# Kernel tuning notes

Measured on AMD Instinct MI355X. Metric: run time of the kernel, lower is better.

## Reference

```python
import jax, jax.numpy as jnp
import numpy as np

NUM_HEADS = 16  # matches init_kwargs num_heads
ROPE_BASE = 10000.0


def _rope(x):
    # x: [B, H, T, d_k]; canonical interleaved rotary embedding
    d = x.shape[-1]
    T = x.shape[-2]
    inv_freq = 1.0 / (ROPE_BASE ** (jnp.arange(0, d, 2, dtype=jnp.float32) / d))  # [d/2]
    ang = jnp.arange(T, dtype=jnp.float32)[:, None] * inv_freq[None, :]  # [T, d/2]
    cos, sin = jnp.cos(ang), jnp.sin(ang)  # broadcast over B,H
    x1 = x[..., 0::2]
    x2 = x[..., 1::2]
    even = x1 * cos - x2 * sin
    odd = x1 * sin + x2 * cos
    return jnp.stack([even, odd], axis=-1).reshape(x.shape)


def setup_inputs() -> dict:
    key = jax.random.key(0)
    ks = jax.random.split(key, 5)
    B, T, D = 2, 2048, 2048
    s = 1.0 / np.sqrt(D)
    return {
        "x": jax.random.normal(ks[0], (B, T, D), dtype=jnp.float32),
        "Wkqv": jax.random.normal(ks[1], (D, 3 * D), dtype=jnp.float32) * s,
        "bkqv": jax.random.normal(ks[2], (3 * D,), dtype=jnp.float32) * 0.01,
        "Wo": jax.random.normal(ks[3], (D, D), dtype=jnp.float32) * s,
        "bo": jax.random.normal(ks[4], (D,), dtype=jnp.float32) * 0.01,
    }


def reference(x, Wkqv, bkqv, Wo, bo):
    B, T, D = x.shape
    H = NUM_HEADS
    d_k = D // H
    kqv = x @ Wkqv + bkqv  # [B, T, 3D]
    # split order per source: index 0 = K, 1 = Q, 2 = V
    k, q, v = jnp.split(kqv, 3, axis=-1)

    def heads(t):  # [B, T, D] -> [B, H, T, d_k]
        return t.reshape(B, T, H, d_k).transpose(0, 2, 1, 3)

    k, q, v = heads(k), heads(q), heads(v)
    k = _rope(k)
    q = _rope(q)
    scores = jnp.einsum('bhtd,bhTd->bhtT', q, k)  # [B, H, T, T]
    causal = jnp.triu(jnp.ones((T, T), dtype=bool), k=1)
    scores = jnp.where(causal, -jnp.inf, scores)
    attn = jax.nn.softmax(scores / jnp.sqrt(jnp.float32(d_k)), axis=-1)
    out = jnp.einsum('bhtT,bhTd->bhtd', attn, v)  # [B, H, T, d_k]
    out = out.transpose(0, 2, 1, 3).reshape(B, T, D)
    return out @ Wo + bo
```

## Files before the change

kernel.cpp:

```cpp
#include <hip/hip_runtime.h>
#include <cstdint>
#include <cstddef>

typedef __attribute__((ext_vector_type(4))) float  floatx4;
typedef __attribute__((ext_vector_type(8))) __bf16 bf16x8;
typedef __attribute__((ext_vector_type(4))) __bf16 bf16x4;

#define B_   2
#define T_   2048
#define D_   2048
#define H_   16
#define DK   128
#define BT_  (B_ * T_)
#define N3   (3 * D_)

__device__ __forceinline__ void async_copy16(const void* g, void* l) {
    __builtin_amdgcn_global_load_lds((const __attribute__((address_space(1))) void*)g,
                                     (__attribute__((address_space(3))) void*)l,
                                     16, 0, 0);
}

__global__ void cast_bf16_kernel(const float* __restrict__ in, __bf16* __restrict__ out, int n4) {
    int i = blockIdx.x * 256 + threadIdx.x;
    if (i >= n4) return;
    float4 v = ((const float4*)in)[i];
    bf16x4 o;
    o.x = (__bf16)v.x; o.y = (__bf16)v.y; o.z = (__bf16)v.z; o.w = (__bf16)v.w;
    ((bf16x4*)out)[i] = o;
}

__global__ void transcast_kernel(const float* __restrict__ in, __bf16* __restrict__ out, int R, int C) {
    __shared__ float tile[32][33];
    int c0 = blockIdx.x * 32, r0 = blockIdx.y * 32;
    int tx = threadIdx.x, ty = threadIdx.y;
#pragma unroll
    for (int j = 0; j < 32; j += 8)
        tile[ty + j][tx] = in[(size_t)(r0 + ty + j) * C + c0 + tx];
    __syncthreads();
#pragma unroll
    for (int j = 0; j < 32; j += 8)
        out[(size_t)(c0 + ty + j) * R + r0 + tx] = (__bf16)tile[tx][ty + j];
}

__global__ void vtrans_kernel(const __bf16* __restrict__ kqv, __bf16* __restrict__ VT) {
    __shared__ __bf16 tile[32][33];
    int bh = blockIdx.z; int b = bh >> 4, h = bh & 15;
    int t0 = blockIdx.x * 32, d0 = blockIdx.y * 32;
    int tx = threadIdx.x, ty = threadIdx.y;
#pragma unroll
    for (int j = 0; j < 32; j += 8)
        tile[ty + j][tx] = kqv[(size_t)(b * T_ + t0 + ty + j) * N3 + 2 * D_ + h * DK + d0 + tx];
    __syncthreads();
#pragma unroll
    for (int j = 0; j < 32; j += 8)
        VT[(size_t)(bh * DK + d0 + ty + j) * T_ + t0 + tx] = tile[tx][ty + j];
}

__global__ void rope_kernel(const __bf16* __restrict__ kqv,
                            __bf16* __restrict__ Kh, __bf16* __restrict__ Qh) {
    int idx = blockIdx.x * 256 + threadIdx.x;
    int i     = idx & 63;
    int t     = (idx >> 6) & (T_ - 1);
    int bh    = (idx >> 17) & 31;
    int which = idx >> 22;
    int b = bh >> 4, h = bh & 15;
    const __bf16* src = kqv + (size_t)(b * T_ + t) * N3 + which * D_ + h * DK + 2 * i;
    float x1 = (float)src[0], x2 = (float)src[1];
    float freq = exp2f((float)i * (-13.287712379549449f / 64.f));
    float ang = (float)t * freq;
    float sn, cn; sincosf(ang, &sn, &cn);
    float s = which ? 0.12751740f : 1.0f;
    __bf16* dst = (which ? Qh : Kh) + (size_t)(bh * T_ + t) * DK + 2 * i;
    dst[0] = (__bf16)((x1 * cn - x2 * sn) * s);
    dst[1] = (__bf16)((x1 * sn + x2 * cn) * s);
}

template <typename OutT>
__global__ __launch_bounds__(256)
void gemm_bt(const __bf16* __restrict__ A, const __bf16* __restrict__ BTm,
             const float* __restrict__ bias, OutT* __restrict__ C,
             int M, int N, int K) {
    __shared__ __align__(16) __bf16 As[128 * 64];
    __shared__ __align__(16) __bf16 Bs[128 * 64];
    const int tid  = threadIdx.x;
    const int lane = tid & 63;
    const int wave = tid >> 6;
    const int quad = lane >> 4;
    const int l16  = lane & 15;
    const int m0 = blockIdx.y * 128;
    const int n0 = blockIdx.x * 128;
    const int wm = (wave & 1) * 64;
    const int wn = (wave >> 1) * 64;

    const floatx4 z4 = {0.f, 0.f, 0.f, 0.f};
    floatx4 acc[4][4];
#pragma unroll
    for (int i = 0; i < 4; ++i)
#pragma unroll
        for (int j = 0; j < 4; ++j) acc[i][j] = z4;

    int           sOff[4];
    const __bf16* gA[4];
    const __bf16* gB[4];
#pragma unroll
    for (int i = 0; i < 4; ++i) {
        int s = i * 256 + tid;
        int row = s >> 3, cs = s & 7;
        int gc = cs ^ (row & 7);
        sOff[i] = s * 8;
        gA[i] = A   + (size_t)(m0 + row) * K + gc * 8;
        gB[i] = BTm + (size_t)(n0 + row) * K + gc * 8;
    }

    for (int kt = 0; kt < K; kt += 64) {
        __syncthreads();
#pragma unroll
        for (int i = 0; i < 4; ++i) {
            async_copy16(gA[i] + kt, As + sOff[i]);
            async_copy16(gB[i] + kt, Bs + sOff[i]);
        }
        __syncthreads();
#pragma unroll
        for (int ks2 = 0; ks2 < 2; ++ks2) {
            bf16x8 af[4], bf[4];
#pragma unroll
            for (int t = 0; t < 4; ++t) {
                int rowA = wm + t * 16 + l16;
                int ca = (ks2 * 4 + quad) ^ (rowA & 7);
                af[t] = *(const bf16x8*)(As + rowA * 64 + ca * 8);
                int rowB = wn + t * 16 + l16;
                int cb = (ks2 * 4 + quad) ^ (rowB & 7);
                bf[t] = *(const bf16x8*)(Bs + rowB * 64 + cb * 8);
            }
#pragma unroll
            for (int mt = 0; mt < 4; ++mt)
#pragma unroll
                for (int nt = 0; nt < 4; ++nt)
                    acc[mt][nt] = __builtin_amdgcn_mfma_f32_16x16x32_bf16(af[mt], bf[nt], acc[mt][nt], 0, 0, 0);
        }
    }

#pragma unroll
    for (int nt = 0; nt < 4; ++nt) {
        int n = n0 + wn + nt * 16 + l16;
        float bv = bias[n];
#pragma unroll
        for (int mt = 0; mt < 4; ++mt)
#pragma unroll
            for (int r = 0; r < 4; ++r) {
                int m = m0 + wm + mt * 16 + quad * 4 + r;
                C[(size_t)m * N + n] = (OutT)(acc[mt][nt][r] + bv);
            }
    }
}

__global__ __launch_bounds__(256)
void fa_kernel(const __bf16* __restrict__ Qg, const __bf16* __restrict__ Kg,
               const __bf16* __restrict__ VTg, __bf16* __restrict__ Og) {
    __shared__ __align__(16) __bf16 Ks[64 * 128];
    __shared__ __align__(16) __bf16 Vs[128 * 64];
    __shared__ __align__(16) __bf16 Ps[4][16 * 64];
    const int tid  = threadIdx.x;
    const int lane = tid & 63, wave = tid >> 6;
    const int quad = lane >> 4, l16 = lane & 15;
    const int bh = blockIdx.y;
    const int j  = blockIdx.x;
    const int b = bh >> 4, h = bh & 15;

    const __bf16* Kb = Kg  + (size_t)bh * T_ * DK;
    const __bf16* Vb = VTg + (size_t)bh * DK * T_;
    __bf16* Psw = Ps[wave];

    const floatx4 z4 = {0.f, 0.f, 0.f, 0.f};

    for (int half = 0; half < 2; ++half) {
        const int qt = half ? (31 - j) : j;
        const int q0 = qt * 64;

        __syncthreads();
        {
            const __bf16* Qb = Qg + (size_t)(bh * T_ + q0) * DK;
#pragma unroll
            for (int i = 0; i < 4; ++i) {
                int s = i * 256 + tid;
                int row = s >> 4, cs = s & 15;
                int gc = cs ^ (row & 7);
                async_copy16(Qb + row * DK + gc * 8, Ks + s * 8);
            }
        }
        __syncthreads();
        bf16x8 qf[4];
#pragma unroll
        for (int ks = 0; ks < 4; ++ks) {
            int row = wave * 16 + l16;
            int c = (ks * 4 + quad) ^ (row & 7);
            qf[ks] = *(const bf16x8*)(Ks + row * DK + c * 8);
        }

        float m_i[4], l_i[4];
        floatx4 accO[8];
#pragma unroll
        for (int r = 0; r < 4; ++r) { m_i[r] = -1e30f; l_i[r] = 0.f; }
#pragma unroll
        for (int nt = 0; nt < 8; ++nt) accO[nt] = z4;

        for (int kt = 0; kt <= qt; ++kt) {
            __syncthreads();
#pragma unroll
            for (int i = 0; i < 4; ++i) {
                int s = i * 256 + tid;
                int row = s >> 4, cs = s & 15;
                int gc = cs ^ (row & 7);
                async_copy16(Kb + (size_t)(kt * 64 + row) * DK + gc * 8, Ks + s * 8);
            }
#pragma unroll
            for (int i = 0; i < 4; ++i) {
                int s = i * 256 + tid;
                int row = s >> 3, cs = s & 7;
                int gc = cs ^ (row & 7);
                async_copy16(Vb + (size_t)row * T_ + kt * 64 + gc * 8, Vs + s * 8);
            }
            __syncthreads();

            floatx4 sc[4];
#pragma unroll
            for (int nt = 0; nt < 4; ++nt) sc[nt] = z4;
#pragma unroll
            for (int ks = 0; ks < 4; ++ks)
#pragma unroll
                for (int nt = 0; nt < 4; ++nt) {
                    int row = nt * 16 + l16;
                    int c = (ks * 4 + quad) ^ (row & 7);
                    bf16x8 kf = *(const bf16x8*)(Ks + row * DK + c * 8);
                    sc[nt] = __builtin_amdgcn_mfma_f32_16x16x32_bf16(qf[ks], kf, sc[nt], 0, 0, 0);
                }

            float mnew[4] = {-1e30f, -1e30f, -1e30f, -1e30f};
            if (kt == qt) {
                const int qrow0 = q0 + wave * 16 + quad * 4;
#pragma unroll
                for (int nt = 0; nt < 4; ++nt) {
                    int kp = kt * 64 + nt * 16 + l16;
#pragma unroll
                    for (int r = 0; r < 4; ++r) {
                        float v = sc[nt][r];
                        v = (kp > qrow0 + r) ? -1e30f : v;
                        sc[nt][r] = v;
                        mnew[r] = fmaxf(mnew[r], v);
                    }
                }
            } else {
#pragma unroll
                for (int nt = 0; nt < 4; ++nt)
#pragma unroll
                    for (int r = 0; r < 4; ++r) mnew[r] = fmaxf(mnew[r], sc[nt][r]);
            }
#pragma unroll
            for (int r = 0; r < 4; ++r) {
                float v = mnew[r];
                v = fmaxf(v, __shfl_xor(v, 1));
                v = fmaxf(v, __shfl_xor(v, 2));
                v = fmaxf(v, __shfl_xor(v, 4));
                v = fmaxf(v, __shfl_xor(v, 8));
                mnew[r] = v;
            }
            float alpha[4];
#pragma unroll
            for (int r = 0; r < 4; ++r) {
                float mi = fmaxf(m_i[r], mnew[r]);
                alpha[r] = exp2f(m_i[r] - mi);
                m_i[r] = mi;
            }
            float rs[4] = {0.f, 0.f, 0.f, 0.f};
#pragma unroll
            for (int nt = 0; nt < 4; ++nt)
#pragma unroll
                for (int r = 0; r < 4; ++r) {
                    float p = exp2f(sc[nt][r] - m_i[r]);
                    sc[nt][r] = p;
                    rs[r] += p;
                }
#pragma unroll
            for (int r = 0; r < 4; ++r) {
                float v = rs[r];
                v += __shfl_xor(v, 1);
                v += __shfl_xor(v, 2);
                v += __shfl_xor(v, 4);
                v += __shfl_xor(v, 8);
                l_i[r] = l_i[r] * alpha[r] + v;
            }
#pragma unroll
            for (int nt = 0; nt < 8; ++nt)
#pragma unroll
                for (int r = 0; r < 4; ++r) accO[nt][r] *= alpha[r];

#pragma unroll
            for (int nt = 0; nt < 4; ++nt) {
                int col = nt * 16 + l16;
                int ch = col >> 3, off = col & 7;
#pragma unroll
                for (int r = 0; r < 4; ++r) {
                    int row = quad * 4 + r;
                    Psw[row * 64 + (ch ^ (row & 7)) * 8 + off] = (__bf16)sc[nt][r];
                }
            }
#pragma unroll
            for (int ks2 = 0; ks2 < 2; ++ks2) {
                int ach = (ks2 * 4 + quad) ^ (l16 & 7);
                bf16x8 pf = *(const bf16x8*)(Psw + l16 * 64 + ach * 8);
#pragma unroll
                for (int nt = 0; nt < 8; ++nt) {
                    int vrow = nt * 16 + l16;
                    int vch = (ks2 * 4 + quad) ^ (vrow & 7);
                    bf16x8 vf = *(const bf16x8*)(Vs + vrow * 64 + vch * 8);
                    accO[nt] = __builtin_amdgcn_mfma_f32_16x16x32_bf16(pf, vf, accO[nt], 0, 0, 0);
                }
            }
        }

#pragma unroll
        for (int nt = 0; nt < 8; ++nt)
#pragma unroll
            for (int r = 0; r < 4; ++r) {
                int trow = q0 + wave * 16 + quad * 4 + r;
                int col = h * DK + nt * 16 + l16;
                Og[(size_t)(b * T_ + trow) * D_ + col] = (__bf16)(accO[nt][r] / l_i[r]);
            }
    }
}

extern "C" void kernel_launch(void* const* d_in, const int* in_sizes, int n_in,
                              void* d_out, int out_size, void* d_ws, size_t ws_size,
                              hipStream_t stream) {
    const float* x    = (const float*)d_in[0];
    const float* Wkqv = (const float*)d_in[1];
    const float* bkqv = (const float*)d_in[2];
    const float* Wo   = (const float*)d_in[3];
    const float* bo   = (const float*)d_in[4];
    float* out = (float*)d_out;

    char* p = (char*)d_ws;
    __bf16* xb    = (__bf16*)p; p += (size_t)BT_ * D_ * 2;
    __bf16* WkqvT = (__bf16*)p; p += (size_t)D_ * N3 * 2;
    __bf16* WoT   = (__bf16*)p; p += (size_t)D_ * D_ * 2;
    __bf16* kqv   = (__bf16*)p; p += (size_t)BT_ * N3 * 2;
    __bf16* qh    = (__bf16*)p; p += (size_t)BT_ * D_ * 2;
    __bf16* kh    = (__bf16*)p; p += (size_t)BT_ * D_ * 2;
    __bf16* vT    = (__bf16*)p; p += (size_t)BT_ * D_ * 2;
    __bf16* ao    = (__bf16*)p; p += (size_t)BT_ * D_ * 2;

    cast_bf16_kernel<<<(BT_ * D_ / 4 + 255) / 256, 256, 0, stream>>>(x, xb, BT_ * D_ / 4);
    transcast_kernel<<<dim3(N3 / 32, D_ / 32), dim3(32, 8), 0, stream>>>(Wkqv, WkqvT, D_, N3);
    transcast_kernel<<<dim3(D_ / 32, D_ / 32), dim3(32, 8), 0, stream>>>(Wo, WoT, D_, D_);
    gemm_bt<__bf16><<<dim3(N3 / 128, BT_ / 128), 256, 0, stream>>>(xb, WkqvT, bkqv, kqv, BT_, N3, D_);
    rope_kernel<<<(2 * 32 * T_ * 64) / 256, 256, 0, stream>>>(kqv, kh, qh);
    vtrans_kernel<<<dim3(T_ / 32, DK / 32, B_ * H_), dim3(32, 8), 0, stream>>>(kqv, vT);
    fa_kernel<<<dim3(16, B_ * H_), 256, 0, stream>>>(qh, kh, vT, ao);
    gemm_bt<float><<<dim3(D_ / 128, BT_ / 128), 256, 0, stream>>>(ao, WoT, bo, out, BT_, D_, D_);
}
```

Measured before the change: 424.2 us.

## Prefetch next K/V tile into registers to overlap loads with compute

Replaces the direct global-to-LDS async copies of K and V tiles with register staging. The next tile is loaded into registers while the current tile is being computed, then written to LDS at the start of the next iteration. Swizzle offsets are precomputed once per thread. This is meant to hide global-memory latency behind the MFMA work, at the cost of extra VGPRs (8 bf16x8 buffers) and explicit LDS stores, which may reduce occupancy.

```diff
diff --git a/kernel.cpp b/kernel.cpp
--- a/kernel.cpp
+++ b/kernel.cpp
@@ -171,6 +171,19 @@
     const __bf16* Vb = VTg + (size_t)bh * DK * T_;
     __bf16* Psw = Ps[wave];
 
+    int    sOffK[4], sOffV[4];
+    size_t gOffK[4], gOffV[4];
+#pragma unroll
+    for (int i = 0; i < 4; ++i) {
+        int s = i * 256 + tid;
+        int rowK = s >> 4, gcK = (s & 15) ^ (rowK & 7);
+        sOffK[i] = s * 8;
+        gOffK[i] = (size_t)rowK * DK + gcK * 8;
+        int rowV = s >> 3, gcV = (s & 7) ^ (rowV & 7);
+        sOffV[i] = s * 8;
+        gOffV[i] = (size_t)rowV * T_ + gcV * 8;
+    }
+
     const floatx4 z4 = {0.f, 0.f, 0.f, 0.f};
 
     for (int half = 0; half < 2; ++half) {
@@ -197,6 +210,13 @@
             qf[ks] = *(const bf16x8*)(Ks + row * DK + c * 8);
         }
 
+        bf16x8 kbuf[4], vbuf[4];
+#pragma unroll
+        for (int i = 0; i < 4; ++i) {
+            kbuf[i] = *(const bf16x8*)(Kb + gOffK[i]);
+            vbuf[i] = *(const bf16x8*)(Vb + gOffV[i]);
+        }
+
         float m_i[4], l_i[4];
         floatx4 accO[8];
 #pragma unroll
@@ -208,19 +228,19 @@
             __syncthreads();
 #pragma unroll
             for (int i = 0; i < 4; ++i) {
-                int s = i * 256 + tid;
-                int row = s >> 4, cs = s & 15;
-                int gc = cs ^ (row & 7);
-                async_copy16(Kb + (size_t)(kt * 64 + row) * DK + gc * 8, Ks + s * 8);
-            }
-#pragma unroll
-            for (int i = 0; i < 4; ++i) {
-                int s = i * 256 + tid;
-                int row = s >> 3, cs = s & 7;
-                int gc = cs ^ (row & 7);
-                async_copy16(Vb + (size_t)row * T_ + kt * 64 + gc * 8, Vs + s * 8);
+                *(bf16x8*)(Ks + sOffK[i]) = kbuf[i];
+                *(bf16x8*)(Vs + sOffV[i]) = vbuf[i];
             }
             __syncthreads();
+            if (kt < qt) {
+                const __bf16* Kn = Kb + (size_t)(kt + 1) * 64 * DK;
+                const __bf16* Vn = Vb + (size_t)(kt + 1) * 64;
+#pragma unroll
+                for (int i = 0; i < 4; ++i) {
+                    kbuf[i] = *(const bf16x8*)(Kn + gOffK[i]);
+                    vbuf[i] = *(const bf16x8*)(Vn + gOffV[i]);
+                }
+            }
 
             floatx4 sc[4];
 #pragma unroll
```

Measured after the change: 458.1 us. +8.0%, slower.

## Double-buffer K/V tiles in flash attention and reuse K buffer for P

Applied to the files above, without the earlier changes.

The attention kernel now keeps two LDS buffers for K/V tiles and issues async loads for the next tile before computing on the current one, so global-to-LDS transfers overlap the MFMA work. The P staging area is overlaid on the consumed K region of the current buffer after a barrier, which keeps LDS usage at 64KB. Address offsets are precomputed once per thread. In exchange it adds an extra barrier per iteration and relies on the async copies being complete by the loop-end syncthreads, which makes correctness depend on waitcnt handling. Higher LDS use may also lower occupancy.

```diff
diff --git a/kernel.cpp b/kernel.cpp
--- a/kernel.cpp
+++ b/kernel.cpp
@@ -157,9 +157,7 @@
 __global__ __launch_bounds__(256)
 void fa_kernel(const __bf16* __restrict__ Qg, const __bf16* __restrict__ Kg,
                const __bf16* __restrict__ VTg, __bf16* __restrict__ Og) {
-    __shared__ __align__(16) __bf16 Ks[64 * 128];
-    __shared__ __align__(16) __bf16 Vs[128 * 64];
-    __shared__ __align__(16) __bf16 Ps[4][16 * 64];
+    __shared__ __align__(16) __bf16 KV[2][16384];
     const int tid  = threadIdx.x;
     const int lane = tid & 63, wave = tid >> 6;
     const int quad = lane >> 4, l16 = lane & 15;
@@ -169,7 +167,19 @@
 
     const __bf16* Kb = Kg  + (size_t)bh * T_ * DK;
     const __bf16* Vb = VTg + (size_t)bh * DK * T_;
-    __bf16* Psw = Ps[wave];
+
+    int    sK[4], sV[4];
+    size_t gK[4], gV[4];
+#pragma unroll
+    for (int i = 0; i < 4; ++i) {
+        int s = i * 256 + tid;
+        int rowK = s >> 4, gcK = (s & 15) ^ (rowK & 7);
+        sK[i] = s * 8;
+        gK[i] = (size_t)rowK * DK + gcK * 8;
+        int rowV = s >> 3, gcV = (s & 7) ^ (rowV & 7);
+        sV[i] = 8192 + s * 8;
+        gV[i] = (size_t)rowV * T_ + gcV * 8;
+    }
 
     const floatx4 z4 = {0.f, 0.f, 0.f, 0.f};
 
@@ -181,12 +191,8 @@
         {
             const __bf16* Qb = Qg + (size_t)(bh * T_ + q0) * DK;
 #pragma unroll
-            for (int i = 0; i < 4; ++i) {
-                int s = i * 256 + tid;
-                int row = s >> 4, cs = s & 15;
-                int gc = cs ^ (row & 7);
-                async_copy16(Qb + row * DK + gc * 8, Ks + s * 8);
-            }
+            for (int i = 0; i < 4; ++i)
+                async_copy16(Qb + gK[i], KV[1] + sK[i]);
         }
         __syncthreads();
         bf16x8 qf[4];
@@ -194,8 +200,14 @@
         for (int ks = 0; ks < 4; ++ks) {
             int row = wave * 16 + l16;
             int c = (ks * 4 + quad) ^ (row & 7);
-            qf[ks] = *(const bf16x8*)(Ks + row * DK + c * 8);
-        }
+            qf[ks] = *(const bf16x8*)(KV[1] + row * DK + c * 8);
+        }
+#pragma unroll
+        for (int i = 0; i < 4; ++i) {
+            async_copy16(Kb + gK[i], KV[0] + sK[i]);
+            async_copy16(Vb + gV[i], KV[0] + sV[i]);
+        }
+        __syncthreads();
 
         float m_i[4], l_i[4];
         floatx4 accO[8];
@@ -205,22 +217,19 @@
         for (int nt = 0; nt < 8; ++nt) accO[nt] = z4;
 
         for (int kt = 0; kt <= qt; ++kt) {
-            __syncthreads();
-#pragma unroll
-            for (int i = 0; i < 4; ++i) {
-                int s = i * 256 + tid;
-                int row = s >> 4, cs = s & 15;
-                int gc = cs ^ (row & 7);
-                async_copy16(Kb + (size_t)(kt * 64 + row) * DK + gc * 8, Ks + s * 8);
-            }
-#pragma unroll
-            for (int i = 0; i < 4; ++i) {
-                int s = i * 256 + tid;
-                int row = s >> 3, cs = s & 7;
-                int gc = cs ^ (row & 7);
-                async_copy16(Vb + (size_t)row * T_ + kt * 64 + gc * 8, Vs + s * 8);
-            }
-            __syncthreads();
+            const int cur = kt & 1;
+            __bf16* bufc = KV[cur];
+            __bf16* bufn = KV[cur ^ 1];
+
+            if (kt < qt) {
+                const __bf16* Kn = Kb + (size_t)(kt + 1) * 64 * DK;
+                const __bf16* Vn = Vb + (size_t)(kt + 1) * 64;
+#pragma unroll
+                for (int i = 0; i < 4; ++i) {
+                    async_copy16(Kn + gK[i], bufn + sK[i]);
+                    async_copy16(Vn + gV[i], bufn + sV[i]);
+                }
+            }
 
             floatx4 sc[4];
 #pragma unroll
@@ -231,7 +240,7 @@
                 for (int nt = 0; nt < 4; ++nt) {
                     int row = nt * 16 + l16;
                     int c = (ks * 4 + quad) ^ (row & 7);
-                    bf16x8 kf = *(const bf16x8*)(Ks + row * DK + c * 8);
+                    bf16x8 kf = *(const bf16x8*)(bufc + row * DK + c * 8);
                     sc[nt] = __builtin_amdgcn_mfma_f32_16x16x32_bf16(qf[ks], kf, sc[nt], 0, 0, 0);
                 }
 
@@ -294,6 +303,9 @@
 #pragma unroll
                 for (int r = 0; r < 4; ++r) accO[nt][r] *= alpha[r];
 
+            asm volatile("s_waitcnt lgkmcnt(0)\n\ts_barrier" ::: "memory");
+
+            __bf16* Pw = bufc + wave * 2048;
 #pragma unroll
             for (int nt = 0; nt < 4; ++nt) {
                 int col = nt * 16 + l16;
@@ -301,21 +313,23 @@
 #pragma unroll
                 for (int r = 0; r < 4; ++r) {
                     int row = quad * 4 + r;
-                    Psw[row * 64 + (ch ^ (row & 7)) * 8 + off] = (__bf16)sc[nt][r];
+                    Pw[row * 64 + (ch ^ (row & 7)) * 8 + off] = (__bf16)sc[nt][r];
                 }
             }
 #pragma unroll
             for (int ks2 = 0; ks2 < 2; ++ks2) {
                 int ach = (ks2 * 4 + quad) ^ (l16 & 7);
-                bf16x8 pf = *(const bf16x8*)(Psw + l16 * 64 + ach * 8);
+                bf16x8 pf = *(const bf16x8*)(Pw + l16 * 64 + ach * 8);
 #pragma unroll
                 for (int nt = 0; nt < 8; ++nt) {
                     int vrow = nt * 16 + l16;
                     int vch = (ks2 * 4 + quad) ^ (vrow & 7);
-                    bf16x8 vf = *(const bf16x8*)(Vs + vrow * 64 + vch * 8);
+                    bf16x8 vf = *(const bf16x8*)(bufc + 8192 + vrow * 64 + vch * 8);
                     accO[nt] = __builtin_amdgcn_mfma_f32_16x16x32_bf16(pf, vf, accO[nt], 0, 0, 0);
                 }
             }
+
+            __syncthreads();
         }
 
 #pragma unroll
```

Result: no change. 425.8 us (+0.4%).
